# Performance work log

Measured on AMD Instinct MI355X. Metric: run time of the kernel, lower is better.

The kernel has to match this reference:

```python
import jax, jax.numpy as jnp
import numpy as np

D_MODEL = 768
EXPAND = 2
D_INNER = EXPAND * D_MODEL  # 1536
D_STATE = 16
D_CONV = 4
DT_RANK = (D_MODEL + 15) // 16  # 48, ceil(d_model/16)
BATCH, SEQ = 8, 2048
EPS = 1e-12


def _silu(x):
    return x * jax.nn.sigmoid(x)


def _mamba(x, in_w, conv_w, conv_b, xproj_w, dt_w, dt_b, A_log, D_skip, out_w):
    # x: (B, L, d_model)
    B, L, _ = x.shape
    xz = x @ in_w.T                      # (B, L, 2*d_inner)
    u, z = jnp.split(xz, 2, axis=-1)     # each (B, L, d_inner)
    # causal depthwise conv1d, kernel D_CONV, left-pad D_CONV-1
    pad = jnp.pad(u, ((0, 0), (D_CONV - 1, 0), (0, 0)))
    uc = conv_b + sum(pad[:, k:k + L, :] * conv_w[:, k] for k in range(D_CONV))
    uc = _silu(uc)                       # (B, L, d_inner)
    x_dbl = uc @ xproj_w.T               # (B, L, dt_rank + 2*d_state)
    dt, Bm, Cm = jnp.split(x_dbl, [DT_RANK, DT_RANK + D_STATE], axis=-1)
    dt = jax.nn.softplus(dt @ dt_w.T + dt_b)  # (B, L, d_inner)
    A = -jnp.exp(A_log)                  # (d_inner, d_state)

    def step(h, t):
        dt_t, B_t, C_t, u_t = t          # (B,di), (B,N), (B,N), (B,di)
        dA = jnp.exp(dt_t[:, :, None] * A)               # (B, di, N)
        h = dA * h + (dt_t * u_t)[:, :, None] * B_t[:, None, :]
        y = jnp.einsum('bdn,bn->bd', h, C_t)
        return h, y

    xs = (dt.swapaxes(0, 1), Bm.swapaxes(0, 1), Cm.swapaxes(0, 1), uc.swapaxes(0, 1))
    h0 = jnp.zeros((B, D_INNER, D_STATE), x.dtype)
    _, ys = jax.lax.scan(step, h0, xs)   # ys: (L, B, d_inner)
    y = ys.swapaxes(0, 1) + uc * D_skip
    return (y * _silu(z)) @ out_w.T      # (B, L, d_model)


def _mamba_params(key):
    ks = jax.random.split(key, 8)
    return dict(
        in_w=jax.random.normal(ks[0], (2 * D_INNER, D_MODEL), jnp.float32) * 0.02,
        conv_w=jax.random.normal(ks[1], (D_INNER, D_CONV), jnp.float32) * 0.2,
        conv_b=jnp.zeros((D_INNER,), jnp.float32),
        xproj_w=jax.random.normal(ks[2], (DT_RANK + 2 * D_STATE, D_INNER), jnp.float32) * 0.02,
        dt_w=jax.random.normal(ks[3], (D_INNER, DT_RANK), jnp.float32) * 0.02,
        dt_b=jax.random.normal(ks[4], (D_INNER,), jnp.float32) * 0.02,
        A_log=jnp.log(jnp.tile(jnp.arange(1, D_STATE + 1, dtype=jnp.float32), (D_INNER, 1))),
        D_skip=jnp.ones((D_INNER,), jnp.float32),
        out_w=jax.random.normal(ks[5], (D_MODEL, D_INNER), jnp.float32) * 0.02,
    )


def setup_inputs() -> dict:
    key = jax.random.key(0)
    k0, k1, k2 = jax.random.split(key, 3)
    inp = {'hidden_states': jax.random.normal(k0, (BATCH, SEQ, D_MODEL), jnp.float32)}
    for pref, k in (('f_', k1), ('b_', k2)):
        for name, v in _mamba_params(k).items():
            inp[pref + name] = v
    inp['ln_g'] = jnp.ones((D_MODEL,), jnp.float32)
    inp['ln_b'] = jnp.zeros((D_MODEL,), jnp.float32)
    return inp


def reference(hidden_states,
              f_in_w, f_conv_w, f_conv_b, f_xproj_w, f_dt_w, f_dt_b, f_A_log, f_D_skip, f_out_w,
              b_in_w, b_conv_w, b_conv_b, b_xproj_w, b_dt_w, b_dt_b, b_A_log, b_D_skip, b_out_w,
              ln_g, ln_b):
    hf = _mamba(hidden_states, f_in_w, f_conv_w, f_conv_b, f_xproj_w, f_dt_w, f_dt_b,
                f_A_log, f_D_skip, f_out_w)
    hb = jnp.flip(_mamba(jnp.flip(hidden_states, 1), b_in_w, b_conv_w, b_conv_b, b_xproj_w,
                         b_dt_w, b_dt_b, b_A_log, b_D_skip, b_out_w), 1)
    h = hf + hb + hidden_states          # dropout is identity at eval
    mu = h.mean(-1, keepdims=True)
    var = ((h - mu) ** 2).mean(-1, keepdims=True)
    return (h - mu) / jnp.sqrt(var + EPS) * ln_g + ln_b
```

## Files before the change

### kernel.cpp

```cpp
#include <hip/hip_runtime.h>
#include <math.h>

#define D_MODEL 768
#define D_INNER 1536
#define D_STATE 16
#define DCONV 4
#define DT_RANK 48
#define BATCH 8
#define SEQ 2048
#define NROWS (BATCH * SEQ)
#define NXZ (2 * D_INNER)
#define NDBC (DT_RANK + 2 * D_STATE)

#define NCHUNK 16
#define CL (SEQ / NCHUNK)
#define NCH (BATCH * D_INNER)
#define DBLKS (D_INNER / 256)
#define KSEG (D_INNER / 4)
#define NP ((size_t)NROWS * NDBC)

#define LOG2E 1.4426950408889634f
#define LN2   0.6931471805599453f

typedef __attribute__((ext_vector_type(8))) short bh8;
typedef __attribute__((ext_vector_type(4))) float f4;
typedef __attribute__((ext_vector_type(8))) unsigned short us8;

__device__ __forceinline__ float bf2f(unsigned short u) {
    return __uint_as_float(((unsigned int)u) << 16);
}
__device__ __forceinline__ unsigned short f2bf(float f) {
    unsigned int x = __float_as_uint(f);
    return (unsigned short)((x + 0x7fffu + ((x >> 16) & 1u)) >> 16);
}
__device__ __forceinline__ float fsigm(float x) {
    return __builtin_amdgcn_rcpf(1.f + __builtin_amdgcn_exp2f(-x * LOG2E));
}

#define GLL16(gp, lp) __builtin_amdgcn_global_load_lds( \
    (const __attribute__((address_space(1))) void*)(gp), \
    (__attribute__((address_space(3))) void*)(lp), 16, 0, 0)

__device__ __forceinline__ void xcd_swizzle(int& bx, int& by) {
    const int nwg = gridDim.x * gridDim.y;
    const int wid = blockIdx.y * gridDim.x + blockIdx.x;
    const int work = (wid & 7) * (nwg >> 3) + (wid >> 3);
    bx = work % gridDim.x;
    by = work / gridDim.x;
}

template <int TC_BF, int ACC, int ACT>
__global__ __launch_bounds__(256) void gemm_mfma(
    const unsigned short* __restrict__ A, int lda,
    const unsigned short* __restrict__ W, int ldw,
    const float* __restrict__ bias,
    void* __restrict__ Cv, int ldc, int K)
{
    __shared__ unsigned short As[128 * 32];
    __shared__ unsigned short Bs[128 * 32];
    int bx, by;
    xcd_swizzle(bx, by);
    const int tid = threadIdx.x;
    const int w = tid >> 6;
    const int l = tid & 63;
    const int wr = w >> 1, wc = w & 1;
    const int tm0 = by * 128;
    const int tn0 = bx * 128;

    const int srow = (w << 4) + (l >> 2);
    const int scol = (l & 3) * 8;
    unsigned short* ldsA0 = &As[(w << 4) * 32];
    unsigned short* ldsA1 = &As[(64 + (w << 4)) * 32];
    unsigned short* ldsB0 = &Bs[(w << 4) * 32];
    unsigned short* ldsB1 = &Bs[(64 + (w << 4)) * 32];
    const unsigned short* gA0 = A + (size_t)(tm0 + srow) * lda + scol;
    const unsigned short* gA1 = A + (size_t)(tm0 + 64 + srow) * lda + scol;
    const unsigned short* gB0 = W + (size_t)(tn0 + srow) * ldw + scol;
    const unsigned short* gB1 = W + (size_t)(tn0 + 64 + srow) * ldw + scol;

    const int aoff = ((wr << 6) + (l & 15)) * 32 + ((l >> 4) << 3);
    const int boff = ((wc << 6) + (l & 15)) * 32 + ((l >> 4) << 3);

    f4 acc[4][4];
#pragma unroll
    for (int i = 0; i < 4; ++i)
#pragma unroll
        for (int j = 0; j < 4; ++j) acc[i][j] = 0.f;

    for (int k0 = 0; k0 < K; k0 += 32) {
        GLL16(gA0 + k0, ldsA0);
        GLL16(gA1 + k0, ldsA1);
        GLL16(gB0 + k0, ldsB0);
        GLL16(gB1 + k0, ldsB1);
        __syncthreads();
        bh8 af[4], bf[4];
#pragma unroll
        for (int mi = 0; mi < 4; ++mi) af[mi] = *(const bh8*)&As[aoff + mi * 512];
#pragma unroll
        for (int ni = 0; ni < 4; ++ni) bf[ni] = *(const bh8*)&Bs[boff + ni * 512];
#pragma unroll
        for (int mi = 0; mi < 4; ++mi)
#pragma unroll
            for (int ni = 0; ni < 4; ++ni)
                acc[mi][ni] = __builtin_amdgcn_mfma_f32_16x16x32_bf16(
                    af[mi], bf[ni], acc[mi][ni], 0, 0, 0);
        __syncthreads();
    }

    const int crow0 = tm0 + (wr << 6) + ((l >> 4) << 2);
    const int ccol0 = tn0 + (wc << 6) + (l & 15);
#pragma unroll
    for (int mi = 0; mi < 4; ++mi)
#pragma unroll
        for (int ni = 0; ni < 4; ++ni)
#pragma unroll
            for (int r = 0; r < 4; ++r) {
                const int n = ccol0 + ni * 16;
                const size_t idx = (size_t)(crow0 + mi * 16 + r) * ldc + n;
                float v = acc[mi][ni][r];
                if (ACT == 1) {
                    v += bias[n];
                    if (v <= 20.f)
                        v = __builtin_amdgcn_logf(1.f + __builtin_amdgcn_exp2f(v * LOG2E)) * LN2;
                }
                if (TC_BF) {
                    ((unsigned short*)Cv)[idx] = f2bf(v);
                } else {
                    float* C = (float*)Cv;
                    C[idx] = ACC ? (C[idx] + v) : v;
                }
            }
}

__global__ __launch_bounds__(256) void gemm_mfma_xp(
    const unsigned short* __restrict__ A, int lda,
    const unsigned short* __restrict__ Wp,
    float* __restrict__ Pp)
{
    __shared__ unsigned short As[128 * 32];
    __shared__ unsigned short Bs[128 * 32];
    int bx, by;
    xcd_swizzle(bx, by);
    const int tid = threadIdx.x;
    const int w = tid >> 6;
    const int l = tid & 63;
    const int wr = w >> 1, wc = w & 1;
    const int tm0 = by * 128;
    const int kbeg = bx * KSEG;

    const int srow = (w << 4) + (l >> 2);
    const int scol = (l & 3) * 8;
    unsigned short* ldsA0 = &As[(w << 4) * 32];
    unsigned short* ldsA1 = &As[(64 + (w << 4)) * 32];
    unsigned short* ldsB0 = &Bs[(w << 4) * 32];
    unsigned short* ldsB1 = &Bs[(64 + (w << 4)) * 32];
    const unsigned short* gA0 = A + (size_t)(tm0 + srow) * lda + scol;
    const unsigned short* gA1 = A + (size_t)(tm0 + 64 + srow) * lda + scol;
    const unsigned short* gB0 = Wp + (size_t)srow * lda + scol;
    const unsigned short* gB1 = Wp + (size_t)(64 + srow) * lda + scol;

    const int aoff = ((wr << 6) + (l & 15)) * 32 + ((l >> 4) << 3);
    const int boff = ((wc << 6) + (l & 15)) * 32 + ((l >> 4) << 3);

    f4 acc[4][4];
#pragma unroll
    for (int i = 0; i < 4; ++i)
#pragma unroll
        for (int j = 0; j < 4; ++j) acc[i][j] = 0.f;

    for (int k0 = kbeg; k0 < kbeg + KSEG; k0 += 32) {
        GLL16(gA0 + k0, ldsA0);
        GLL16(gA1 + k0, ldsA1);
        GLL16(gB0 + k0, ldsB0);
        GLL16(gB1 + k0, ldsB1);
        __syncthreads();
        bh8 af[4], bf[4];
#pragma unroll
        for (int mi = 0; mi < 4; ++mi) af[mi] = *(const bh8*)&As[aoff + mi * 512];
#pragma unroll
        for (int ni = 0; ni < 4; ++ni) bf[ni] = *(const bh8*)&Bs[boff + ni * 512];
#pragma unroll
        for (int mi = 0; mi < 4; ++mi)
#pragma unroll
            for (int ni = 0; ni < 4; ++ni)
                acc[mi][ni] = __builtin_amdgcn_mfma_f32_16x16x32_bf16(
                    af[mi], bf[ni], acc[mi][ni], 0, 0, 0);
        __syncthreads();
    }

    const int crow0 = tm0 + (wr << 6) + ((l >> 4) << 2);
    const int ccol0 = (wc << 6) + (l & 15);
    float* pdst = Pp + (size_t)bx * NP;
#pragma unroll
    for (int mi = 0; mi < 4; ++mi)
#pragma unroll
        for (int ni = 0; ni < 4; ++ni) {
            const int n = ccol0 + ni * 16;
            if (n >= 80) continue;
#pragma unroll
            for (int r = 0; r < 4; ++r) {
                const int m = crow0 + mi * 16 + r;
                pdst[(size_t)m * NDBC + n] = acc[mi][ni][r];
            }
        }
}

__global__ __launch_bounds__(256) void xp_reduce(
    const float* __restrict__ Pp, float* __restrict__ dtBC,
    unsigned short* __restrict__ dtR)
{
    const size_t i = (size_t)blockIdx.x * 256 + threadIdx.x;
    const float s = (Pp[i] + Pp[i + NP]) + (Pp[i + 2 * NP] + Pp[i + 3 * NP]);
    dtBC[i] = s;
    const int n = (int)(i % NDBC);
    if (n < 64) {
        const size_t m = i / NDBC;
        dtR[m * 64 + n] = f2bf(s);
    }
}

__global__ __launch_bounds__(256) void cast_f32_bf16(
    const float* __restrict__ in, unsigned short* __restrict__ out, int n4)
{
    const int i = blockIdx.x * 256 + threadIdx.x;
    if (i >= n4) return;
    const float4 v = ((const float4*)in)[i];
    ushort4 o;
    o.x = f2bf(v.x); o.y = f2bf(v.y); o.z = f2bf(v.z); o.w = f2bf(v.w);
    ((ushort4*)out)[i] = o;
}

__global__ __launch_bounds__(256) void cast_dtw(
    const float* __restrict__ in, unsigned short* __restrict__ out)
{
    const int i = blockIdx.x * 256 + threadIdx.x;
    if (i >= D_INNER * 64) return;
    const int d = i >> 6, k = i & 63;
    out[i] = (k < DT_RANK) ? f2bf(in[d * DT_RANK + k]) : (unsigned short)0;
}

template <int DIR>
__global__ __launch_bounds__(256) void conv_silu8(
    const unsigned short* __restrict__ xz, const float* __restrict__ conv_w,
    const float* __restrict__ conv_b, unsigned short* __restrict__ uc)
{
    const int idx = blockIdx.x * 256 + threadIdx.x;
    const int row = idx / 192;
    const int dp  = (idx - row * 192) * 8;
    const int l = row & (SEQ - 1);

    f4 cw[8];
#pragma unroll
    for (int i = 0; i < 8; ++i)
        cw[i] = *(const f4*)&conv_w[(dp + i) * 4];

    float acc[8];
    {
        const f4 b0 = *(const f4*)&conv_b[dp];
        const f4 b1 = *(const f4*)&conv_b[dp + 4];
#pragma unroll
        for (int i = 0; i < 4; ++i) { acc[i] = b0[i]; acc[4 + i] = b1[i]; }
    }

#pragma unroll
    for (int j = 0; j < 4; ++j) {
        const int ll = DIR ? (l + j) : (l - j);
        if (ll >= 0 && ll < SEQ) {
            const us8 v = *(const us8*)&xz[((long)row + (ll - l)) * NXZ + dp];
#pragma unroll
            for (int i = 0; i < 8; ++i)
                acc[i] = fmaf(bf2f(v[i]), cw[i][3 - j], acc[i]);
        }
    }
    us8 o;
#pragma unroll
    for (int i = 0; i < 8; ++i)
        o[i] = f2bf(acc[i] * fsigm(acc[i]));
    *(us8*)&uc[(size_t)row * D_INNER + dp] = o;
}

template <int DIR>
__global__ __launch_bounds__(256) void scan1_d(
    const float* __restrict__ dtBC, const unsigned short* __restrict__ uc,
    const float* __restrict__ A_log, const unsigned short* __restrict__ xz,
    float* __restrict__ Fb, float* __restrict__ Sd)
{
    __shared__ float bs[CL][20];
    const int tid = threadIdx.x;
    const int c    = blockIdx.x / (DBLKS * BATCH);
    const int rem  = blockIdx.x % (DBLKS * BATCH);
    const int b    = rem / DBLKS;
    const int dblk = rem % DBLKS;
    const int d = dblk * 256 + tid;
    const long l0 = DIR ? (SEQ - 1 - c * CL) : (c * CL);

    {
        const int rk = tid >> 1, half = tid & 1;
        const long l = DIR ? (l0 - rk) : (l0 + rk);
        const float* src = &dtBC[((size_t)b * SEQ + l) * NDBC + DT_RANK + half * 8];
        *(f4*)&bs[rk][half * 8]     = *(const f4*)src;
        *(f4*)&bs[rk][half * 8 + 4] = *(const f4*)(src + 4);
    }
    __syncthreads();

    float A2[16];
#pragma unroll
    for (int n = 0; n < 16; ++n)
        A2[n] = -expf(A_log[d * D_STATE + n]) * LOG2E;

    const unsigned short* pdt = xz + (size_t)b * SEQ * NXZ + d;
    const unsigned short* pu  = uc + (size_t)b * SEQ * D_INNER + d;

    float h[16];
#pragma unroll
    for (int n = 0; n < 16; ++n) h[n] = 0.f;
    float sdt = 0.f;

    float dt8a[8], u8a[8], dt8b[8], u8b[8];
    auto LOAD = [&](float* dt8, float* u8, int k0) {
#pragma unroll
        for (int j = 0; j < 8; ++j) {
            const long l = DIR ? (l0 - (k0 + j)) : (l0 + (k0 + j));
            dt8[j] = bf2f(pdt[l * NXZ]);
            u8[j]  = bf2f(pu[l * D_INNER]);
        }
    };
    auto COMP = [&](const float* dt8, const float* u8, int k0) {
#pragma unroll
        for (int j = 0; j < 8; ++j) {
            const float dt = dt8[j];
            const float dtu = dt * u8[j];
            sdt += dt;
            const int k = k0 + j;
#pragma unroll
            for (int q = 0; q < 4; ++q) {
                const f4 Bq = *(const f4*)&bs[k][q * 4];
#pragma unroll
                for (int e = 0; e < 4; ++e) {
                    const int n = q * 4 + e;
                    const float dA = __builtin_amdgcn_exp2f(dt * A2[n]);
                    h[n] = fmaf(dA, h[n], dtu * Bq[e]);
                }
            }
        }
    };
    LOAD(dt8a, u8a, 0);
    for (int k0 = 0; k0 < CL; k0 += 16) {
        LOAD(dt8b, u8b, k0 + 8);
        COMP(dt8a, u8a, k0);
        if (k0 + 16 < CL) LOAD(dt8a, u8a, k0 + 16);
        COMP(dt8b, u8b, k0 + 8);
    }

    const int ch = b * D_INNER + d;
    float* fdst = Fb + ((size_t)c * NCH + ch) * 16;
#pragma unroll
    for (int n = 0; n < 16; ++n) fdst[n] = h[n];
    Sd[(size_t)c * NCH + ch] = sdt;
}

__global__ __launch_bounds__(256) void scan_comb(
    float* __restrict__ Fb, const float* __restrict__ Sd,
    const float* __restrict__ A_log)
{
    const int i = blockIdx.x * 256 + threadIdx.x;
    const int ch = i >> 4, n = i & 15;
    const int d = ch % D_INNER;
    const float A2 = -expf(A_log[d * D_STATE + n]) * LOG2E;
    float h = Fb[i];
    for (int cc = 1; cc < NCHUNK - 1; ++cc) {
        const float P = __builtin_amdgcn_exp2f(A2 * Sd[(size_t)cc * NCH + ch]);
        h = fmaf(P, h, Fb[(size_t)cc * (NCH * 16) + i]);
        Fb[(size_t)cc * (NCH * 16) + i] = h;
    }
}

template <int DIR>
__global__ __launch_bounds__(256) void scan2_d(
    const float* __restrict__ dtBC, const unsigned short* __restrict__ uc,
    const float* __restrict__ A_log, const float* __restrict__ D_skip,
    unsigned short* __restrict__ xz, const float* __restrict__ Fb)
{
    __shared__ float bs[CL][36];
    const int tid = threadIdx.x;
    const int c    = blockIdx.x / (DBLKS * BATCH);
    const int rem  = blockIdx.x % (DBLKS * BATCH);
    const int b    = rem / DBLKS;
    const int dblk = rem % DBLKS;
    const int d = dblk * 256 + tid;
    const long l0 = DIR ? (SEQ - 1 - c * CL) : (c * CL);

    {
        const int rk = tid >> 1, half = tid & 1;
        const long l = DIR ? (l0 - rk) : (l0 + rk);
        const float* src = &dtBC[((size_t)b * SEQ + l) * NDBC + DT_RANK + half * 16];
        *(f4*)&bs[rk][half * 16]      = *(const f4*)src;
        *(f4*)&bs[rk][half * 16 + 4]  = *(const f4*)(src + 4);
        *(f4*)&bs[rk][half * 16 + 8]  = *(const f4*)(src + 8);
        *(f4*)&bs[rk][half * 16 + 12] = *(const f4*)(src + 12);
    }
    __syncthreads();

    float A2[16];
#pragma unroll
    for (int n = 0; n < 16; ++n)
        A2[n] = -expf(A_log[d * D_STATE + n]) * LOG2E;
    const float Dv = D_skip[d];

    const unsigned short* pdt = xz + (size_t)b * SEQ * NXZ + d;
    const unsigned short* pz  = pdt + D_INNER;
    const unsigned short* pu  = uc + (size_t)b * SEQ * D_INNER + d;
    unsigned short* pout = xz + (size_t)b * SEQ * NXZ + d;

    const int ch = b * D_INNER + d;
    float h[16];
    if (c == 0) {
#pragma unroll
        for (int n = 0; n < 16; ++n) h[n] = 0.f;
    } else {
        const float* hsrc = Fb + ((size_t)(c - 1) * NCH + ch) * 16;
#pragma unroll
        for (int n = 0; n < 16; ++n) h[n] = hsrc[n];
    }

    float dt8a[8], u8a[8], z8a[8], dt8b[8], u8b[8], z8b[8];
    auto LOAD = [&](float* dt8, float* u8, float* z8, int k0) {
#pragma unroll
        for (int j = 0; j < 8; ++j) {
            const long l = DIR ? (l0 - (k0 + j)) : (l0 + (k0 + j));
            dt8[j] = bf2f(pdt[l * NXZ]);
            u8[j]  = bf2f(pu[l * D_INNER]);
            z8[j]  = bf2f(pz[l * NXZ]);
        }
    };
    auto COMP = [&](const float* dt8, const float* u8, const float* z8, int k0) {
#pragma unroll
        for (int j = 0; j < 8; ++j) {
            const float dt = dt8[j];
            const float dtu = dt * u8[j];
            float ya[4];
            ya[0] = u8[j] * Dv; ya[1] = 0.f; ya[2] = 0.f; ya[3] = 0.f;
            const int k = k0 + j;
#pragma unroll
            for (int q = 0; q < 4; ++q) {
                const f4 Bq = *(const f4*)&bs[k][q * 4];
                const f4 Cq = *(const f4*)&bs[k][16 + q * 4];
#pragma unroll
                for (int e = 0; e < 4; ++e) {
                    const int n = q * 4 + e;
                    const float dA = __builtin_amdgcn_exp2f(dt * A2[n]);
                    h[n] = fmaf(dA, h[n], dtu * Bq[e]);
                    ya[e] = fmaf(h[n], Cq[e], ya[e]);
                }
            }
            const float y = (ya[0] + ya[1]) + (ya[2] + ya[3]);
            const float zv = z8[j];
            const long l = DIR ? (l0 - k) : (l0 + k);
            pout[l * NXZ] = f2bf(y * (zv * fsigm(zv)));
        }
    };
    LOAD(dt8a, u8a, z8a, 0);
    for (int k0 = 0; k0 < CL; k0 += 16) {
        LOAD(dt8b, u8b, z8b, k0 + 8);
        COMP(dt8a, u8a, z8a, k0);
        if (k0 + 16 < CL) LOAD(dt8a, u8a, z8a, k0 + 16);
        COMP(dt8b, u8b, z8b, k0 + 8);
    }
}

__global__ __launch_bounds__(256) void fuse_ln(
    float* __restrict__ out, const float* __restrict__ x,
    const float* __restrict__ g, const float* __restrict__ bta)
{
    const int row = blockIdx.x;
    const size_t base = (size_t)row * D_MODEL;
    float vals[3];
    float s = 0.f, s2 = 0.f;
#pragma unroll
    for (int i = 0; i < 3; ++i) {
        const int c = threadIdx.x + i * 256;
        const float v = out[base + c] + x[base + c];
        vals[i] = v;
        s += v;
        s2 += v * v;
    }
#pragma unroll
    for (int o = 32; o >= 1; o >>= 1) {
        s  += __shfl_xor(s, o, 64);
        s2 += __shfl_xor(s2, o, 64);
    }
    __shared__ float ls[4], ls2[4];
    const int wid = threadIdx.x >> 6;
    if ((threadIdx.x & 63) == 0) { ls[wid] = s; ls2[wid] = s2; }
    __syncthreads();
    s  = ls[0] + ls[1] + ls[2] + ls[3];
    s2 = ls2[0] + ls2[1] + ls2[2] + ls2[3];
    const float mu  = s * (1.f / D_MODEL);
    const float var = s2 * (1.f / D_MODEL) - mu * mu;
    const float inv = 1.f / sqrtf(var + 1e-12f);
#pragma unroll
    for (int i = 0; i < 3; ++i) {
        const int c = threadIdx.x + i * 256;
        out[base + c] = (vals[i] - mu) * inv * g[c] + bta[c];
    }
}

extern "C" void kernel_launch(void* const* d_in, const int* in_sizes, int n_in,
                              void* d_out, int out_size, void* d_ws, size_t ws_size,
                              hipStream_t stream)
{
    const float* x = (const float*)d_in[0];
    const float* ln_g = (const float*)d_in[19];
    const float* ln_b = (const float*)d_in[20];

    float* dtBC = (float*)d_ws;
    unsigned short* xz  = (unsigned short*)(dtBC + (size_t)NROWS * NDBC);
    unsigned short* uc  = xz + (size_t)NROWS * NXZ;
    unsigned short* xbf = uc + (size_t)NROWS * D_INNER;
    unsigned short* wbf_in  = xbf + (size_t)NROWS * D_MODEL;
    unsigned short* wbf_out = wbf_in + (size_t)NXZ * D_MODEL;
    unsigned short* wbf_xp  = wbf_out + (size_t)D_MODEL * D_INNER;
    unsigned short* dtw_pad = wbf_xp + (size_t)128 * D_INNER;
    unsigned short* dtR     = dtw_pad + (size_t)D_INNER * 64;
    float* Fb = (float*)(dtR + (size_t)NROWS * 64);
    float* Sd = Fb + (size_t)(NCHUNK - 1) * NCH * 16;
    float* Pp = Sd + (size_t)(NCHUNK - 1) * NCH;
    const size_t needed = ((size_t)NROWS * NDBC) * 4
        + ((size_t)NROWS * NXZ + (size_t)NROWS * D_INNER + (size_t)NROWS * D_MODEL
           + (size_t)NXZ * D_MODEL + (size_t)D_MODEL * D_INNER
           + (size_t)128 * D_INNER + (size_t)D_INNER * 64 + (size_t)NROWS * 64) * 2
        + (size_t)(NCHUNK - 1) * NCH * 16 * 4
        + (size_t)(NCHUNK - 1) * NCH * 4
        + 4 * NP * 4;
    if (ws_size < needed) return;

    float* outp = (float*)d_out;

    cast_f32_bf16<<<(NROWS * D_MODEL / 4 + 255) / 256, 256, 0, stream>>>(
        x, xbf, NROWS * D_MODEL / 4);

    for (int dir = 0; dir < 2; ++dir) {
        const float* in_w    = (const float*)d_in[1 + dir * 9 + 0];
        const float* conv_w  = (const float*)d_in[1 + dir * 9 + 1];
        const float* conv_b  = (const float*)d_in[1 + dir * 9 + 2];
        const float* xproj_w = (const float*)d_in[1 + dir * 9 + 3];
        const float* dt_w    = (const float*)d_in[1 + dir * 9 + 4];
        const float* dt_b    = (const float*)d_in[1 + dir * 9 + 5];
        const float* A_log   = (const float*)d_in[1 + dir * 9 + 6];
        const float* D_skip  = (const float*)d_in[1 + dir * 9 + 7];
        const float* out_w   = (const float*)d_in[1 + dir * 9 + 8];

        cast_f32_bf16<<<(NXZ * D_MODEL / 4 + 255) / 256, 256, 0, stream>>>(
            in_w, wbf_in, NXZ * D_MODEL / 4);
        cast_f32_bf16<<<(D_MODEL * D_INNER / 4 + 255) / 256, 256, 0, stream>>>(
            out_w, wbf_out, D_MODEL * D_INNER / 4);
        cast_f32_bf16<<<(NDBC * D_INNER / 4 + 255) / 256, 256, 0, stream>>>(
            xproj_w, wbf_xp, NDBC * D_INNER / 4);
        cast_dtw<<<(D_INNER * 64 + 255) / 256, 256, 0, stream>>>(dt_w, dtw_pad);

        gemm_mfma<1, 0, 0><<<dim3(NXZ / 128, NROWS / 128), 256, 0, stream>>>(
            xbf, D_MODEL, wbf_in, D_MODEL, nullptr, xz, NXZ, D_MODEL);

        if (dir == 0)
            conv_silu8<0><<<NROWS * 192 / 256, 256, 0, stream>>>(
                xz, conv_w, conv_b, uc);
        else
            conv_silu8<1><<<NROWS * 192 / 256, 256, 0, stream>>>(
                xz, conv_w, conv_b, uc);

        gemm_mfma_xp<<<dim3(4, NROWS / 128), 256, 0, stream>>>(
            uc, D_INNER, wbf_xp, Pp);
        xp_reduce<<<(int)(NP / 256), 256, 0, stream>>>(Pp, dtBC, dtR);

        gemm_mfma<1, 0, 1><<<dim3(D_INNER / 128, NROWS / 128), 256, 0, stream>>>(
            dtR, 64, dtw_pad, 64, dt_b, xz, NXZ, 64);

        if (dir == 0) {
            scan1_d<0><<<(NCHUNK - 1) * DBLKS * BATCH, 256, 0, stream>>>(
                dtBC, uc, A_log, xz, Fb, Sd);
            scan_comb<<<NCH * 16 / 256, 256, 0, stream>>>(Fb, Sd, A_log);
            scan2_d<0><<<NCHUNK * DBLKS * BATCH, 256, 0, stream>>>(
                dtBC, uc, A_log, D_skip, xz, Fb);
        } else {
            scan1_d<1><<<(NCHUNK - 1) * DBLKS * BATCH, 256, 0, stream>>>(
                dtBC, uc, A_log, xz, Fb, Sd);
            scan_comb<<<NCH * 16 / 256, 256, 0, stream>>>(Fb, Sd, A_log);
            scan2_d<1><<<NCHUNK * DBLKS * BATCH, 256, 0, stream>>>(
                dtBC, uc, A_log, D_skip, xz, Fb);
        }

        if (dir == 0)
            gemm_mfma<0, 0, 0><<<dim3(D_MODEL / 128, NROWS / 128), 256, 0, stream>>>(
                xz, NXZ, wbf_out, D_INNER, nullptr, outp, D_MODEL, D_INNER);
        else
            gemm_mfma<0, 1, 0><<<dim3(D_MODEL / 128, NROWS / 128), 256, 0, stream>>>(
                xz, NXZ, wbf_out, D_INNER, nullptr, outp, D_MODEL, D_INNER);
    }

    fuse_ln<<<NROWS, 256, 0, stream>>>(outp, x, ln_g, ln_b);
}
```

Baseline: 951.7 us.

## Double GEMM K-tile with XOR-swizzled LDS, more scan chunks, fuse weight casts

The MFMA GEMMs now stage 64-wide K tiles with an XOR-swizzled LDS layout. This halves the number of barrier iterations and is meant to avoid LDS bank conflicts; the XCD block swizzle is dropped. The scan chunk count doubles from 16 to 32 for more parallelism, and the three weight-cast kernels merge into one launch. The x-proj partial buffer now aliases the scan carry buffer, which shrinks the workspace but relies on the two not being live at the same time.

```diff
diff --git a/kernel.cpp b/kernel.cpp
--- a/kernel.cpp
+++ b/kernel.cpp
@@ -12,7 +12,7 @@
 #define NXZ (2 * D_INNER)
 #define NDBC (DT_RANK + 2 * D_STATE)
 
-#define NCHUNK 16
+#define NCHUNK 32
 #define CL (SEQ / NCHUNK)
 #define NCH (BATCH * D_INNER)
 #define DBLKS (D_INNER / 256)
@@ -40,14 +40,6 @@
 #define GLL16(gp, lp) __builtin_amdgcn_global_load_lds( \
     (const __attribute__((address_space(1))) void*)(gp), \
     (__attribute__((address_space(3))) void*)(lp), 16, 0, 0)
-
-__device__ __forceinline__ void xcd_swizzle(int& bx, int& by) {
-    const int nwg = gridDim.x * gridDim.y;
-    const int wid = blockIdx.y * gridDim.x + blockIdx.x;
-    const int work = (wid & 7) * (nwg >> 3) + (wid >> 3);
-    bx = work % gridDim.x;
-    by = work / gridDim.x;
-}
 
 template <int TC_BF, int ACC, int ACT>
 __global__ __launch_bounds__(256) void gemm_mfma(
@@ -56,30 +48,31 @@
     const float* __restrict__ bias,
     void* __restrict__ Cv, int ldc, int K)
 {
-    __shared__ unsigned short As[128 * 32];
-    __shared__ unsigned short Bs[128 * 32];
-    int bx, by;
-    xcd_swizzle(bx, by);
+    __shared__ unsigned short As[128 * 64];
+    __shared__ unsigned short Bs[128 * 64];
     const int tid = threadIdx.x;
     const int w = tid >> 6;
     const int l = tid & 63;
     const int wr = w >> 1, wc = w & 1;
-    const int tm0 = by * 128;
-    const int tn0 = bx * 128;
-
-    const int srow = (w << 4) + (l >> 2);
-    const int scol = (l & 3) * 8;
-    unsigned short* ldsA0 = &As[(w << 4) * 32];
-    unsigned short* ldsA1 = &As[(64 + (w << 4)) * 32];
-    unsigned short* ldsB0 = &Bs[(w << 4) * 32];
-    unsigned short* ldsB1 = &Bs[(64 + (w << 4)) * 32];
-    const unsigned short* gA0 = A + (size_t)(tm0 + srow) * lda + scol;
-    const unsigned short* gA1 = A + (size_t)(tm0 + 64 + srow) * lda + scol;
-    const unsigned short* gB0 = W + (size_t)(tn0 + srow) * ldw + scol;
-    const unsigned short* gB1 = W + (size_t)(tn0 + 64 + srow) * ldw + scol;
-
-    const int aoff = ((wr << 6) + (l & 15)) * 32 + ((l >> 4) << 3);
-    const int boff = ((wc << 6) + (l & 15)) * 32 + ((l >> 4) << 3);
+    const int tm0 = blockIdx.y * 128;
+    const int tn0 = blockIdx.x * 128;
+
+    const int srow = (w << 3) + (l >> 3);
+    const int scol = (((l & 7) ^ (l >> 3)) << 3);
+    const unsigned short* gAi[4];
+    const unsigned short* gBi[4];
+    unsigned short* lAi[4];
+    unsigned short* lBi[4];
+#pragma unroll
+    for (int i = 0; i < 4; ++i) {
+        gAi[i] = A + (size_t)(tm0 + i * 32 + srow) * lda + scol;
+        gBi[i] = W + (size_t)(tn0 + i * 32 + srow) * ldw + scol;
+        lAi[i] = &As[(i * 32 + (w << 3)) * 64];
+        lBi[i] = &Bs[(i * 32 + (w << 3)) * 64];
+    }
+
+    const int arow = (wr << 6) + (l & 15);
+    const int brow = (wc << 6) + (l & 15);
 
     f4 acc[4][4];
 #pragma unroll
@@ -87,23 +80,30 @@
 #pragma unroll
         for (int j = 0; j < 4; ++j) acc[i][j] = 0.f;
 
-    for (int k0 = 0; k0 < K; k0 += 32) {
-        GLL16(gA0 + k0, ldsA0);
-        GLL16(gA1 + k0, ldsA1);
-        GLL16(gB0 + k0, ldsB0);
-        GLL16(gB1 + k0, ldsB1);
+    for (int k0 = 0; k0 < K; k0 += 64) {
+#pragma unroll
+        for (int i = 0; i < 4; ++i) {
+            GLL16(gAi[i] + k0, lAi[i]);
+            GLL16(gBi[i] + k0, lBi[i]);
+        }
         __syncthreads();
-        bh8 af[4], bf[4];
-#pragma unroll
-        for (int mi = 0; mi < 4; ++mi) af[mi] = *(const bh8*)&As[aoff + mi * 512];
-#pragma unroll
-        for (int ni = 0; ni < 4; ++ni) bf[ni] = *(const bh8*)&Bs[boff + ni * 512];
-#pragma unroll
-        for (int mi = 0; mi < 4; ++mi)
+#pragma unroll
+        for (int ks = 0; ks < 2; ++ks) {
+            const int kc = ((ks << 2) + (l >> 4)) ^ (l & 7);
+            bh8 af[4], bf[4];
+#pragma unroll
+            for (int mi = 0; mi < 4; ++mi)
+                af[mi] = *(const bh8*)&As[(arow + mi * 16) * 64 + kc * 8];
 #pragma unroll
             for (int ni = 0; ni < 4; ++ni)
-                acc[mi][ni] = __builtin_amdgcn_mfma_f32_16x16x32_bf16(
-                    af[mi], bf[ni], acc[mi][ni], 0, 0, 0);
+                bf[ni] = *(const bh8*)&Bs[(brow + ni * 16) * 64 + kc * 8];
+#pragma unroll
+            for (int mi = 0; mi < 4; ++mi)
+#pragma unroll
+                for (int ni = 0; ni < 4; ++ni)
+                    acc[mi][ni] = __builtin_amdgcn_mfma_f32_16x16x32_bf16(
+                        af[mi], bf[ni], acc[mi][ni], 0, 0, 0);
+        }
         __syncthreads();
     }
 
@@ -137,30 +137,32 @@
     const unsigned short* __restrict__ Wp,
     float* __restrict__ Pp)
 {
-    __shared__ unsigned short As[128 * 32];
-    __shared__ unsigned short Bs[128 * 32];
-    int bx, by;
-    xcd_swizzle(bx, by);
+    __shared__ unsigned short As[128 * 64];
+    __shared__ unsigned short Bs[128 * 64];
     const int tid = threadIdx.x;
     const int w = tid >> 6;
     const int l = tid & 63;
     const int wr = w >> 1, wc = w & 1;
-    const int tm0 = by * 128;
-    const int kbeg = bx * KSEG;
-
-    const int srow = (w << 4) + (l >> 2);
-    const int scol = (l & 3) * 8;
-    unsigned short* ldsA0 = &As[(w << 4) * 32];
-    unsigned short* ldsA1 = &As[(64 + (w << 4)) * 32];
-    unsigned short* ldsB0 = &Bs[(w << 4) * 32];
-    unsigned short* ldsB1 = &Bs[(64 + (w << 4)) * 32];
-    const unsigned short* gA0 = A + (size_t)(tm0 + srow) * lda + scol;
-    const unsigned short* gA1 = A + (size_t)(tm0 + 64 + srow) * lda + scol;
-    const unsigned short* gB0 = Wp + (size_t)srow * lda + scol;
-    const unsigned short* gB1 = Wp + (size_t)(64 + srow) * lda + scol;
-
-    const int aoff = ((wr << 6) + (l & 15)) * 32 + ((l >> 4) << 3);
-    const int boff = ((wc << 6) + (l & 15)) * 32 + ((l >> 4) << 3);
+    const int kseg = blockIdx.x;
+    const int tm0 = blockIdx.y * 128;
+    const int kbeg = kseg * KSEG;
+
+    const int srow = (w << 3) + (l >> 3);
+    const int scol = (((l & 7) ^ (l >> 3)) << 3);
+    const unsigned short* gAi[4];
+    const unsigned short* gBi[4];
+    unsigned short* lAi[4];
+    unsigned short* lBi[4];
+#pragma unroll
+    for (int i = 0; i < 4; ++i) {
+        gAi[i] = A + (size_t)(tm0 + i * 32 + srow) * lda + scol;
+        gBi[i] = Wp + (size_t)(i * 32 + srow) * lda + scol;
+        lAi[i] = &As[(i * 32 + (w << 3)) * 64];
+        lBi[i] = &Bs[(i * 32 + (w << 3)) * 64];
+    }
+
+    const int arow = (wr << 6) + (l & 15);
+    const int brow = (wc << 6) + (l & 15);
 
     f4 acc[4][4];
 #pragma unroll
@@ -168,29 +170,36 @@
 #pragma unroll
         for (int j = 0; j < 4; ++j) acc[i][j] = 0.f;
 
-    for (int k0 = kbeg; k0 < kbeg + KSEG; k0 += 32) {
-        GLL16(gA0 + k0, ldsA0);
-        GLL16(gA1 + k0, ldsA1);
-        GLL16(gB0 + k0, ldsB0);
-        GLL16(gB1 + k0, ldsB1);
+    for (int k0 = kbeg; k0 < kbeg + KSEG; k0 += 64) {
+#pragma unroll
+        for (int i = 0; i < 4; ++i) {
+            GLL16(gAi[i] + k0, lAi[i]);
+            GLL16(gBi[i] + k0, lBi[i]);
+        }
         __syncthreads();
-        bh8 af[4], bf[4];
-#pragma unroll
-        for (int mi = 0; mi < 4; ++mi) af[mi] = *(const bh8*)&As[aoff + mi * 512];
-#pragma unroll
-        for (int ni = 0; ni < 4; ++ni) bf[ni] = *(const bh8*)&Bs[boff + ni * 512];
-#pragma unroll
-        for (int mi = 0; mi < 4; ++mi)
+#pragma unroll
+        for (int ks = 0; ks < 2; ++ks) {
+            const int kc = ((ks << 2) + (l >> 4)) ^ (l & 7);
+            bh8 af[4], bf[4];
+#pragma unroll
+            for (int mi = 0; mi < 4; ++mi)
+                af[mi] = *(const bh8*)&As[(arow + mi * 16) * 64 + kc * 8];
 #pragma unroll
             for (int ni = 0; ni < 4; ++ni)
-                acc[mi][ni] = __builtin_amdgcn_mfma_f32_16x16x32_bf16(
-                    af[mi], bf[ni], acc[mi][ni], 0, 0, 0);
+                bf[ni] = *(const bh8*)&Bs[(brow + ni * 16) * 64 + kc * 8];
+#pragma unroll
+            for (int mi = 0; mi < 4; ++mi)
+#pragma unroll
+                for (int ni = 0; ni < 4; ++ni)
+                    acc[mi][ni] = __builtin_amdgcn_mfma_f32_16x16x32_bf16(
+                        af[mi], bf[ni], acc[mi][ni], 0, 0, 0);
+        }
         __syncthreads();
     }
 
     const int crow0 = tm0 + (wr << 6) + ((l >> 4) << 2);
     const int ccol0 = (wc << 6) + (l & 15);
-    float* pdst = Pp + (size_t)bx * NP;
+    float* pdst = Pp + (size_t)kseg * NP;
 #pragma unroll
     for (int mi = 0; mi < 4; ++mi)
 #pragma unroll
@@ -228,6 +237,27 @@
     ushort4 o;
     o.x = f2bf(v.x); o.y = f2bf(v.y); o.z = f2bf(v.z); o.w = f2bf(v.w);
     ((ushort4*)out)[i] = o;
+}
+
+#define N4_IN  (NXZ * D_MODEL / 4)
+#define N4_OUT (D_MODEL * D_INNER / 4)
+#define N4_XP  (NDBC * D_INNER / 4)
+__global__ __launch_bounds__(256) void cast_w3(
+    const float* __restrict__ in_w, const float* __restrict__ out_w,
+    const float* __restrict__ xp_w, unsigned short* __restrict__ o_in,
+    unsigned short* __restrict__ o_out, unsigned short* __restrict__ o_xp)
+{
+    int i = blockIdx.x * 256 + threadIdx.x;
+    const float* src;
+    unsigned short* dst;
+    if (i < N4_IN) { src = in_w; dst = o_in; }
+    else if (i < N4_IN + N4_OUT) { src = out_w; dst = o_out; i -= N4_IN; }
+    else if (i < N4_IN + N4_OUT + N4_XP) { src = xp_w; dst = o_xp; i -= N4_IN + N4_OUT; }
+    else return;
+    const float4 v = ((const float4*)src)[i];
+    ushort4 o;
+    o.x = f2bf(v.x); o.y = f2bf(v.y); o.z = f2bf(v.z); o.w = f2bf(v.w);
+    ((ushort4*)dst)[i] = o;
 }
 
 __global__ __launch_bounds__(256) void cast_dtw(
@@ -294,7 +324,7 @@
     const int d = dblk * 256 + tid;
     const long l0 = DIR ? (SEQ - 1 - c * CL) : (c * CL);
 
-    {
+    if (tid < 2 * CL) {
         const int rk = tid >> 1, half = tid & 1;
         const long l = DIR ? (l0 - rk) : (l0 + rk);
         const float* src = &dtBC[((size_t)b * SEQ + l) * NDBC + DT_RANK + half * 8];
@@ -390,7 +420,7 @@
     const int d = dblk * 256 + tid;
     const long l0 = DIR ? (SEQ - 1 - c * CL) : (c * CL);
 
-    {
+    if (tid < 2 * CL) {
         const int rk = tid >> 1, half = tid & 1;
         const long l = DIR ? (l0 - rk) : (l0 + rk);
         const float* src = &dtBC[((size_t)b * SEQ + l) * NDBC + DT_RANK + half * 16];
@@ -523,15 +553,14 @@
     unsigned short* dtw_pad = wbf_xp + (size_t)128 * D_INNER;
     unsigned short* dtR     = dtw_pad + (size_t)D_INNER * 64;
     float* Fb = (float*)(dtR + (size_t)NROWS * 64);
+    float* Pp = Fb;
     float* Sd = Fb + (size_t)(NCHUNK - 1) * NCH * 16;
-    float* Pp = Sd + (size_t)(NCHUNK - 1) * NCH;
     const size_t needed = ((size_t)NROWS * NDBC) * 4
         + ((size_t)NROWS * NXZ + (size_t)NROWS * D_INNER + (size_t)NROWS * D_MODEL
            + (size_t)NXZ * D_MODEL + (size_t)D_MODEL * D_INNER
            + (size_t)128 * D_INNER + (size_t)D_INNER * 64 + (size_t)NROWS * 64) * 2
         + (size_t)(NCHUNK - 1) * NCH * 16 * 4
-        + (size_t)(NCHUNK - 1) * NCH * 4
-        + 4 * NP * 4;
+        + (size_t)(NCHUNK - 1) * NCH * 4;
     if (ws_size < needed) return;
 
     float* outp = (float*)d_out;
@@ -550,12 +579,8 @@
         const float* D_skip  = (const float*)d_in[1 + dir * 9 + 7];
         const float* out_w   = (const float*)d_in[1 + dir * 9 + 8];
 
-        cast_f32_bf16<<<(NXZ * D_MODEL / 4 + 255) / 256, 256, 0, stream>>>(
-            in_w, wbf_in, NXZ * D_MODEL / 4);
-        cast_f32_bf16<<<(D_MODEL * D_INNER / 4 + 255) / 256, 256, 0, stream>>>(
-            out_w, wbf_out, D_MODEL * D_INNER / 4);
-        cast_f32_bf16<<<(NDBC * D_INNER / 4 + 255) / 256, 256, 0, stream>>>(
-            xproj_w, wbf_xp, NDBC * D_INNER / 4);
+        cast_w3<<<(N4_IN + N4_OUT + N4_XP + 255) / 256, 256, 0, stream>>>(
+            in_w, out_w, xproj_w, wbf_in, wbf_out, wbf_xp);
         cast_dtw<<<(D_INNER * 64 + 255) / 256, 256, 0, stream>>>(dt_w, dtw_pad);
 
         gemm_mfma<1, 0, 0><<<dim3(NXZ / 128, NROWS / 128), 256, 0, stream>>>(
```

Measured after the change: 962.9 us. About the same (+1.2%).
